# Performance work log

Hardware: AMD Instinct MI355X
Metric: run time of the kernel (lower is better)

## Reference

```python
import jax, jax.numpy as jnp
import numpy as np

N_NODES = 50000
IN_CH = 128
HID_CH = 256
N_EDGES = 800000

def setup_inputs() -> dict:
    key = jax.random.key(0)
    k1, k2, k3, k4, k5 = jax.random.split(key, 5)
    x = jax.random.normal(k1, (N_NODES, IN_CH), dtype=jnp.float32)
    edge_index = jax.random.randint(k2, (2, N_EDGES), 0, N_NODES, dtype=jnp.int64)
    # SAGEConv params: lin_l (applied to aggregated neighbors, has bias), lin_r (applied to root, no bias)
    s = 1.0 / np.sqrt(IN_CH)
    W_l = jax.random.uniform(k3, (IN_CH, HID_CH), dtype=jnp.float32, minval=-s, maxval=s)
    b_l = jnp.zeros((HID_CH,), dtype=jnp.float32)
    W_r = jax.random.uniform(k4, (IN_CH, HID_CH), dtype=jnp.float32, minval=-s, maxval=s)
    return {"x": x, "edge_index": edge_index, "W_l": W_l, "b_l": b_l, "W_r": W_r}

def reference(x, edge_index, W_l, b_l, W_r):
    src, dst = edge_index[0], edge_index[1]
    # gather source features along edges, scatter-mean into destination nodes
    msgs = x[src]  # [E, in]
    agg_sum = jax.ops.segment_sum(msgs, dst, num_segments=N_NODES)  # [N, in]
    deg = jax.ops.segment_sum(jnp.ones((N_EDGES,), x.dtype), dst, num_segments=N_NODES)
    agg = agg_sum / jnp.maximum(deg, 1.0)[:, None]
    # SAGEConv: lin_l(aggregated) + lin_r(root), then ReLU
    out = agg @ W_l + b_l + x @ W_r
    return jax.nn.relu(out)
```

## Files before the change

kernel.cpp:

```cpp
#include <hip/hip_runtime.h>
#include <hip/hip_bf16.h>

#define IN_CH   128
#define HID_CH  256
#define KTOT    256

#define BUCK_NODES 128
#define NBUCK      391
#define BUCK_CAP   2432
#define SCHUNK     4096

typedef __attribute__((ext_vector_type(8))) short bf16x8;
typedef __attribute__((ext_vector_type(4))) float f32x4;
typedef __attribute__((ext_vector_type(2))) float f32x2;

static __device__ __forceinline__ unsigned short f2bf(float f) {
    unsigned int u = __float_as_uint(f);
    unsigned int r = (u + 0x7FFFu + ((u >> 16) & 1u)) >> 16;
    return (unsigned short)r;
}
static __device__ __forceinline__ float bf2f(unsigned int ubits16) {
    return __uint_as_float(ubits16 << 16);
}

static __device__ __forceinline__ void gload_lds16(const void* g, void* l) {
    __builtin_amdgcn_global_load_lds(
        (const __attribute__((address_space(1))) void*)g,
        (__attribute__((address_space(3))) void*)l, 16, 0, 0);
}

static __device__ __forceinline__ unsigned enc_e4m3(float f) {
    unsigned u = __float_as_uint(f);
    unsigned s = (u >> 24) & 0x80u;
    float af = fabsf(f);
    if (af >= 448.f) return s | 0x7Eu;
    if (af < 0.0009765625f) return s;
    if (af < 0.015625f) {
        int m = (int)(af * 512.0f + 0.5f);
        if (m > 7) return s | 0x08u;
        return s | (unsigned)m;
    }
    unsigned au = u & 0x7fffffffu;
    unsigned r = au + 0x0007FFFFu + ((au >> 20) & 1u);
    unsigned e8 = r >> 23;
    unsigned m = (r >> 20) & 7u;
    int e4 = (int)e8 - 120;
    if (e4 >= 16) return s | 0x7Eu;
    return s | ((unsigned)e4 << 3) | m;
}

static __device__ __forceinline__ void dec4_e4m3(unsigned v, float& c0, float& c1,
                                                 float& c2, float& c3) {
#if __has_builtin(__builtin_amdgcn_cvt_pk_f32_fp8)
    f32x2 dlo = __builtin_amdgcn_cvt_pk_f32_fp8(v, false);
    f32x2 dhi = __builtin_amdgcn_cvt_pk_f32_fp8(v, true);
    c0 = dlo.x; c1 = dlo.y; c2 = dhi.x; c3 = dhi.y;
#else
    unsigned b[4] = {v & 0xFFu, (v >> 8) & 0xFFu, (v >> 16) & 0xFFu, v >> 24};
    float o[4];
    #pragma unroll
    for (int i = 0; i < 4; ++i) {
        unsigned e = (b[i] >> 3) & 15u, m = b[i] & 7u;
        unsigned nz = (e != 0u) ? 1u : 0u;
        float val = (float)(m + (nz << 3)) * __uint_as_float((e + 117u + (1u - nz)) << 23);
        o[i] = (b[i] & 0x80u) ? -val : val;
    }
    c0 = o[0]; c1 = o[1]; c2 = o[2]; c3 = o[3];
#endif
}

__global__ __launch_bounds__(1024) void front_kernel(
    const float* __restrict__ x, const int* __restrict__ ei,
    const float* __restrict__ Wl, const float* __restrict__ Wr,
    unsigned short* __restrict__ featb, unsigned char* __restrict__ fx8,
    unsigned short* __restrict__ WT, int* __restrict__ histg,
    int N, int Npad, int E, int nchunk, int nxb)
{
    __shared__ int h[NBUCK];
    const int b = blockIdx.x, tid = threadIdx.x;

    if (b < 64) {
        int t = b * 1024 + tid;
        int n = t >> 8, k = t & 255;
        float v = (k < IN_CH) ? Wl[(size_t)k * HID_CH + n]
                              : Wr[(size_t)(k - IN_CH) * HID_CH + n];
        WT[(size_t)n * KTOT + k] = f2bf(v);
        return;
    }
    if (b < 64 + nxb) {
        int t = (b - 64) * 1024 + tid;
        if (t >= Npad * 16) return;
        int n = t >> 4, c8 = (t & 15) * 8;
        if (n >= N) {
            uint4 z = {0u, 0u, 0u, 0u};
            *reinterpret_cast<uint4*>(featb + (size_t)n * KTOT + c8) = z;
            *reinterpret_cast<uint4*>(featb + (size_t)n * KTOT + IN_CH + c8) = z;
            uint2 z2 = {0u, 0u};
            *reinterpret_cast<uint2*>(fx8 + (size_t)n * IN_CH + c8) = z2;
            return;
        }
        const float* src = x + (size_t)n * IN_CH + c8;
        float4 v0 = *reinterpret_cast<const float4*>(src);
        float4 v1 = *reinterpret_cast<const float4*>(src + 4);
        uint4 o;
        o.x = (unsigned)f2bf(v0.x) | ((unsigned)f2bf(v0.y) << 16);
        o.y = (unsigned)f2bf(v0.z) | ((unsigned)f2bf(v0.w) << 16);
        o.z = (unsigned)f2bf(v1.x) | ((unsigned)f2bf(v1.y) << 16);
        o.w = (unsigned)f2bf(v1.z) | ((unsigned)f2bf(v1.w) << 16);
        *reinterpret_cast<uint4*>(featb + (size_t)n * KTOT + IN_CH + c8) = o;
        uint2 p;
        p.x = enc_e4m3(v0.x) | (enc_e4m3(v0.y) << 8) |
              (enc_e4m3(v0.z) << 16) | (enc_e4m3(v0.w) << 24);
        p.y = enc_e4m3(v1.x) | (enc_e4m3(v1.y) << 8) |
              (enc_e4m3(v1.z) << 16) | (enc_e4m3(v1.w) << 24);
        *reinterpret_cast<uint2*>(fx8 + (size_t)n * IN_CH + c8) = p;
        return;
    }
    int c = b - 64 - nxb;
    if (tid < NBUCK) h[tid] = 0;
    __syncthreads();
    #pragma unroll
    for (int r = 0; r < SCHUNK / 1024; ++r) {
        int i = c * SCHUNK + r * 1024 + tid;
        if (i < E) atomicAdd(&h[((unsigned)ei[E + i]) >> 7], 1);
    }
    __syncthreads();
    if (tid < NBUCK) histg[(size_t)tid * nchunk + c] = h[tid];
}

__global__ __launch_bounds__(1024) void rowscan_kernel(
    int* __restrict__ histg, int* __restrict__ btot, int nchunk)
{
    __shared__ int s[1024];
    const int b = blockIdx.x, t = threadIdx.x;
    int v = (t < nchunk) ? histg[(size_t)b * nchunk + t] : 0;
    s[t] = v;
    __syncthreads();
    #pragma unroll
    for (int off = 1; off < 1024; off <<= 1) {
        int add = (t >= off) ? s[t - off] : 0;
        __syncthreads();
        s[t] += add;
        __syncthreads();
    }
    if (t < nchunk) histg[(size_t)b * nchunk + t] = s[t] - v;
    if (t == 1023) btot[b] = s[1023];
}

__global__ __launch_bounds__(1024) void scatter_part_kernel(
    const int* __restrict__ ei, const int* __restrict__ histg,
    const int* __restrict__ btot, unsigned* __restrict__ barr,
    int E, int nchunk)
{
    __shared__ unsigned stagr[SCHUNK];
    __shared__ unsigned stag[SCHUNK];
    __shared__ unsigned short bidr[SCHUNK];
    __shared__ unsigned short bid[SCHUNK];
    __shared__ int lh[NBUCK];
    __shared__ int lstart[NBUCK];
    __shared__ int lc[NBUCK];
    __shared__ int ls[512];
    __shared__ int sb[512];

    const int c = blockIdx.x, tid = threadIdx.x;
    const int e0 = c * SCHUNK;
    const int nval = min(SCHUNK, E - e0);

    if (tid < NBUCK) lh[tid] = 0;
    if (tid < 512) sb[tid] = (tid < NBUCK) ? btot[tid] : 0;
    __syncthreads();

    #pragma unroll
    for (int r = 0; r < SCHUNK / 1024; ++r) {
        int li = r * 1024 + tid;
        if (li < nval) {
            int i = e0 + li;
            unsigned src = (unsigned)ei[i];
            unsigned dst = (unsigned)ei[E + i];
            unsigned bkt = dst >> 7;
            stagr[li] = src | ((dst & 127u) << 16);
            bidr[li] = (unsigned short)bkt;
            atomicAdd(&lh[bkt], 1);
        }
    }
    __syncthreads();
    #pragma unroll
    for (int off = 1; off < 512; off <<= 1) {
        int add = (tid < 512 && tid >= off) ? sb[tid - off] : 0;
        __syncthreads();
        if (tid < 512) sb[tid] += add;
        __syncthreads();
    }
    if (tid < 512) ls[tid] = (tid < NBUCK) ? lh[tid] : 0;
    __syncthreads();
    #pragma unroll
    for (int off = 1; off < 512; off <<= 1) {
        int add = (tid < 512 && tid >= off) ? ls[tid - off] : 0;
        __syncthreads();
        if (tid < 512) ls[tid] += add;
        __syncthreads();
    }
    if (tid < NBUCK) {
        int st = ls[tid] - lh[tid];
        lstart[tid] = st;
        lc[tid] = 0;
    }
    __syncthreads();

    #pragma unroll
    for (int r = 0; r < SCHUNK / 1024; ++r) {
        int li = r * 1024 + tid;
        if (li < nval) {
            unsigned bkt = bidr[li];
            int pos = lstart[bkt] + atomicAdd(&lc[bkt], 1);
            stag[pos] = stagr[li];
            bid[pos] = (unsigned short)bkt;
        }
    }
    __syncthreads();

    #pragma unroll
    for (int r = 0; r < SCHUNK / 1024; ++r) {
        int li = r * 1024 + tid;
        if (li < nval) {
            unsigned bkt = bid[li];
            int gbase = histg[(size_t)bkt * nchunk + c] +
                        ((bkt == 0) ? 0 : sb[bkt - 1]);
            barr[(size_t)gbase + (li - lstart[bkt])] = stag[li];
        }
    }
}

__global__ __launch_bounds__(1024) void fused_gather_kernel(
    const unsigned* __restrict__ barr, const int* __restrict__ btot,
    const unsigned char* __restrict__ fx8, unsigned short* __restrict__ featb,
    int N)
{
    __shared__ unsigned s_edge[BUCK_CAP];
    __shared__ unsigned short s_col[BUCK_CAP];
    __shared__ int s_cnt[BUCK_NODES];
    __shared__ int s_start[BUCK_NODES];
    __shared__ int s_cur[BUCK_NODES];
    __shared__ int s_scan[BUCK_NODES];
    __shared__ int sb[512];

    const int b = blockIdx.x;
    const int tid = threadIdx.x;
    const int node0 = b * BUCK_NODES;
    const int nnodes = min(BUCK_NODES, N - node0);

    if (tid < 512) sb[tid] = (tid < NBUCK) ? btot[tid] : 0;
    if (tid < BUCK_NODES) s_cnt[tid] = 0;
    __syncthreads();
    #pragma unroll
    for (int off = 1; off < 512; off <<= 1) {
        int add = (tid < 512 && tid >= off) ? sb[tid - off] : 0;
        __syncthreads();
        if (tid < 512) sb[tid] += add;
        __syncthreads();
    }
    const int base = (b == 0) ? 0 : sb[b - 1];
    int nb = btot[b];
    nb = (nb < BUCK_CAP) ? nb : BUCK_CAP;

    for (int i = tid; i < nb; i += 1024) {
        unsigned p = barr[(size_t)base + i];
        s_edge[i] = p;
        atomicAdd(&s_cnt[p >> 16], 1);
    }
    __syncthreads();

    if (tid < BUCK_NODES) s_scan[tid] = s_cnt[tid];
    __syncthreads();
    #pragma unroll
    for (int off = 1; off < BUCK_NODES; off <<= 1) {
        int add = 0;
        if (tid < BUCK_NODES && tid >= off) add = s_scan[tid - off];
        __syncthreads();
        if (tid < BUCK_NODES) s_scan[tid] += add;
        __syncthreads();
    }
    if (tid < BUCK_NODES) {
        int st = s_scan[tid] - s_cnt[tid];
        s_start[tid] = st;
        s_cur[tid] = st;
    }
    __syncthreads();

    for (int i = tid; i < nb; i += 1024) {
        unsigned p = s_edge[i];
        int pos = atomicAdd(&s_cur[p >> 16], 1);
        s_col[pos] = (unsigned short)(p & 0xFFFFu);
    }
    __syncthreads();

    const int wid = tid >> 6, lane = tid & 63;
    const int q4 = lane >> 4, sub = lane & 15;
    for (int pr = wid; pr < BUCK_NODES / 4; pr += 16) {
        int ln = pr * 4 + q4;
        bool live = (ln < nnodes);
        int deg = live ? s_cnt[ln] : 0;
        int beg = live ? s_start[ln] : 0;
        float a0 = 0.f, a1 = 0.f, a2 = 0.f, a3 = 0.f;
        float a4 = 0.f, a5 = 0.f, a6 = 0.f, a7 = 0.f;
        for (int e = 0; e < deg; e += 8) {
            uint2 vv[8];
            #pragma unroll
            for (int q = 0; q < 8; ++q) {
                int ee = e + q;
                ee = (ee < deg) ? ee : (deg - 1);
                int s = s_col[beg + ee];
                vv[q] = *reinterpret_cast<const uint2*>(
                    fx8 + (size_t)s * IN_CH + sub * 8);
            }
            #pragma unroll
            for (int q = 0; q < 8; ++q) {
                float m = (e + q < deg) ? 1.f : 0.f;
                float c0, c1, c2, c3, c4, c5, c6, c7;
                dec4_e4m3(vv[q].x, c0, c1, c2, c3);
                dec4_e4m3(vv[q].y, c4, c5, c6, c7);
                a0 = fmaf(m, c0, a0); a1 = fmaf(m, c1, a1);
                a2 = fmaf(m, c2, a2); a3 = fmaf(m, c3, a3);
                a4 = fmaf(m, c4, a4); a5 = fmaf(m, c5, a5);
                a6 = fmaf(m, c6, a6); a7 = fmaf(m, c7, a7);
            }
        }
        if (live) {
            float inv = 1.0f / fmaxf((float)deg, 1.0f);
            uint4 o;
            o.x = (unsigned)f2bf(a0 * inv) | ((unsigned)f2bf(a1 * inv) << 16);
            o.y = (unsigned)f2bf(a2 * inv) | ((unsigned)f2bf(a3 * inv) << 16);
            o.z = (unsigned)f2bf(a4 * inv) | ((unsigned)f2bf(a5 * inv) << 16);
            o.w = (unsigned)f2bf(a6 * inv) | ((unsigned)f2bf(a7 * inv) << 16);
            *reinterpret_cast<uint4*>(
                featb + (size_t)(node0 + ln) * KTOT + sub * 8) = o;
        }
    }
}

__global__ __launch_bounds__(256, 2) void sage_mfma_kernel(
    const unsigned short* __restrict__ featb,
    const unsigned short* __restrict__ WT,
    const float* __restrict__ bl,
    float* __restrict__ out, int N)
{
    __shared__ unsigned short sA[128][64];
    __shared__ unsigned short sB[256][64];

    const int tid   = threadIdx.x;
    const int nbase = blockIdx.x * 128;
    const int lane  = tid & 63;
    const int w     = tid >> 6;
    const int wr    = (w >> 1) * 64;
    const int wc    = (w & 1) * 128;
    const int lr    = lane & 15;
    const int lk    = (lane >> 4) * 8;
    const int srow  = lane >> 3;
    const int scol  = (lane & 7) * 8;

    f32x4 acc[4][8] = {};

    for (int kb = 0; kb < KTOT; kb += 64) {
        __syncthreads();
        #pragma unroll
        for (int p = 0; p < 4; ++p) {
            int r0 = (w + p * 4) * 8;
            gload_lds16(featb + (size_t)(nbase + r0 + srow) * KTOT + kb + scol,
                        &sA[r0][0]);
        }
        #pragma unroll
        for (int p = 0; p < 8; ++p) {
            int r0 = (w + p * 4) * 8;
            gload_lds16(WT + (size_t)(r0 + srow) * KTOT + kb + scol,
                        &sB[r0][0]);
        }
        __syncthreads();
        #pragma unroll
        for (int ks = 0; ks < 2; ++ks) {
            bf16x8 af[4], bfr[8];
            #pragma unroll
            for (int i = 0; i < 4; ++i)
                af[i] = *reinterpret_cast<const bf16x8*>(&sA[wr + i * 16 + lr][ks * 32 + lk]);
            #pragma unroll
            for (int i = 0; i < 8; ++i)
                bfr[i] = *reinterpret_cast<const bf16x8*>(&sB[wc + i * 16 + lr][ks * 32 + lk]);
            #pragma unroll
            for (int mi = 0; mi < 4; ++mi)
                #pragma unroll
                for (int ni = 0; ni < 8; ++ni)
                    acc[mi][ni] = __builtin_amdgcn_mfma_f32_16x16x32_bf16(
                        af[mi], bfr[ni], acc[mi][ni], 0, 0, 0);
        }
    }

    #pragma unroll
    for (int ni = 0; ni < 8; ++ni) {
        float bias = bl[wc + ni * 16 + lr];
        #pragma unroll
        for (int mi = 0; mi < 4; ++mi) {
            #pragma unroll
            for (int r = 0; r < 4; ++r) {
                int row = nbase + wr + mi * 16 + (lane >> 4) * 4 + r;
                if (row < N) {
                    int colj = wc + ni * 16 + lr;
                    out[(size_t)row * HID_CH + colj] = fmaxf(acc[mi][ni][r] + bias, 0.0f);
                }
            }
        }
    }
}

extern "C" void kernel_launch(void* const* d_in, const int* in_sizes, int n_in,
                              void* d_out, int out_size, void* d_ws, size_t ws_size,
                              hipStream_t stream) {
    const float* x  = (const float*)d_in[0];
    const int*   ei = (const int*)d_in[1];
    const float* Wl = (const float*)d_in[2];
    const float* bl = (const float*)d_in[3];
    const float* Wr = (const float*)d_in[4];
    float* out = (float*)d_out;

    const int N = in_sizes[0] / IN_CH;
    const int E = in_sizes[1] / 2;
    const int Npad   = ((N + 127) / 128) * 128;
    const int nchunk = (E + SCHUNK - 1) / SCHUNK;
    const int nxb    = (Npad * 16 + 1023) / 1024;

    unsigned short* featb = (unsigned short*)d_ws;
    unsigned short* WT    = featb + (size_t)Npad * KTOT;
    unsigned char*  fx8   = (unsigned char*)(WT + KTOT * HID_CH);
    unsigned* barr = (unsigned*)(fx8 + (size_t)Npad * IN_CH);
    int* histg = (int*)(barr + E);
    int* btot  = histg + (size_t)NBUCK * nchunk;

    front_kernel<<<64 + nxb + nchunk, 1024, 0, stream>>>(
        x, ei, Wl, Wr, featb, fx8, WT, histg, N, Npad, E, nchunk, nxb);
    rowscan_kernel<<<NBUCK, 1024, 0, stream>>>(histg, btot, nchunk);
    scatter_part_kernel<<<nchunk, 1024, 0, stream>>>(ei, histg, btot, barr, E, nchunk);
    fused_gather_kernel<<<NBUCK, 1024, 0, stream>>>(barr, btot, fx8, featb, N);
    sage_mfma_kernel<<<Npad / 128, 256, 0, stream>>>(featb, WT, bl, out, N);
}
```

Measured before the change: 79.90 us.

## Replace histogram+rowscan bucket partition with atomic fixed-capacity bucket slots

Removes the per-chunk destination histogram pass and the row-scan kernel, so edges go straight into fixed-capacity per-bucket slots. Each scatter block claims space in a bucket with one global atomicAdd on a per-bucket cursor, which front_kernel zeroes. This cuts one kernel launch, one full read of the destination indices, and the repeated prefix scans over bucket totals. In exchange, edge order within a bucket becomes nondeterministic, and edges beyond BUCK_CAP per bucket are silently dropped, which the code before also truncated.

```diff
diff --git a/kernel.cpp b/kernel.cpp
--- a/kernel.cpp
+++ b/kernel.cpp
@@ -70,16 +70,16 @@
 }
 
 __global__ __launch_bounds__(1024) void front_kernel(
-    const float* __restrict__ x, const int* __restrict__ ei,
+    const float* __restrict__ x,
     const float* __restrict__ Wl, const float* __restrict__ Wr,
     unsigned short* __restrict__ featb, unsigned char* __restrict__ fx8,
-    unsigned short* __restrict__ WT, int* __restrict__ histg,
-    int N, int Npad, int E, int nchunk, int nxb)
+    unsigned short* __restrict__ WT, int* __restrict__ gcur,
+    int N, int Npad)
 {
-    __shared__ int h[NBUCK];
     const int b = blockIdx.x, tid = threadIdx.x;
 
     if (b < 64) {
+        if (b == 0 && tid < NBUCK) gcur[tid] = 0;
         int t = b * 1024 + tid;
         int n = t >> 8, k = t & 255;
         float v = (k < IN_CH) ? Wl[(size_t)k * HID_CH + n]
@@ -87,70 +87,37 @@
         WT[(size_t)n * KTOT + k] = f2bf(v);
         return;
     }
-    if (b < 64 + nxb) {
-        int t = (b - 64) * 1024 + tid;
-        if (t >= Npad * 16) return;
-        int n = t >> 4, c8 = (t & 15) * 8;
-        if (n >= N) {
-            uint4 z = {0u, 0u, 0u, 0u};
-            *reinterpret_cast<uint4*>(featb + (size_t)n * KTOT + c8) = z;
-            *reinterpret_cast<uint4*>(featb + (size_t)n * KTOT + IN_CH + c8) = z;
-            uint2 z2 = {0u, 0u};
-            *reinterpret_cast<uint2*>(fx8 + (size_t)n * IN_CH + c8) = z2;
-            return;
-        }
-        const float* src = x + (size_t)n * IN_CH + c8;
-        float4 v0 = *reinterpret_cast<const float4*>(src);
-        float4 v1 = *reinterpret_cast<const float4*>(src + 4);
-        uint4 o;
-        o.x = (unsigned)f2bf(v0.x) | ((unsigned)f2bf(v0.y) << 16);
-        o.y = (unsigned)f2bf(v0.z) | ((unsigned)f2bf(v0.w) << 16);
-        o.z = (unsigned)f2bf(v1.x) | ((unsigned)f2bf(v1.y) << 16);
-        o.w = (unsigned)f2bf(v1.z) | ((unsigned)f2bf(v1.w) << 16);
-        *reinterpret_cast<uint4*>(featb + (size_t)n * KTOT + IN_CH + c8) = o;
-        uint2 p;
-        p.x = enc_e4m3(v0.x) | (enc_e4m3(v0.y) << 8) |
-              (enc_e4m3(v0.z) << 16) | (enc_e4m3(v0.w) << 24);
-        p.y = enc_e4m3(v1.x) | (enc_e4m3(v1.y) << 8) |
-              (enc_e4m3(v1.z) << 16) | (enc_e4m3(v1.w) << 24);
-        *reinterpret_cast<uint2*>(fx8 + (size_t)n * IN_CH + c8) = p;
+    int t = (b - 64) * 1024 + tid;
+    if (t >= Npad * 16) return;
+    int n = t >> 4, c8 = (t & 15) * 8;
+    if (n >= N) {
+        uint4 z = {0u, 0u, 0u, 0u};
+        *reinterpret_cast<uint4*>(featb + (size_t)n * KTOT + c8) = z;
+        *reinterpret_cast<uint4*>(featb + (size_t)n * KTOT + IN_CH + c8) = z;
+        uint2 z2 = {0u, 0u};
+        *reinterpret_cast<uint2*>(fx8 + (size_t)n * IN_CH + c8) = z2;
         return;
     }
-    int c = b - 64 - nxb;
-    if (tid < NBUCK) h[tid] = 0;
-    __syncthreads();
-    #pragma unroll
-    for (int r = 0; r < SCHUNK / 1024; ++r) {
-        int i = c * SCHUNK + r * 1024 + tid;
-        if (i < E) atomicAdd(&h[((unsigned)ei[E + i]) >> 7], 1);
-    }
-    __syncthreads();
-    if (tid < NBUCK) histg[(size_t)tid * nchunk + c] = h[tid];
-}
-
-__global__ __launch_bounds__(1024) void rowscan_kernel(
-    int* __restrict__ histg, int* __restrict__ btot, int nchunk)
-{
-    __shared__ int s[1024];
-    const int b = blockIdx.x, t = threadIdx.x;
-    int v = (t < nchunk) ? histg[(size_t)b * nchunk + t] : 0;
-    s[t] = v;
-    __syncthreads();
-    #pragma unroll
-    for (int off = 1; off < 1024; off <<= 1) {
-        int add = (t >= off) ? s[t - off] : 0;
-        __syncthreads();
-        s[t] += add;
-        __syncthreads();
-    }
-    if (t < nchunk) histg[(size_t)b * nchunk + t] = s[t] - v;
-    if (t == 1023) btot[b] = s[1023];
+    const float* src = x + (size_t)n * IN_CH + c8;
+    float4 v0 = *reinterpret_cast<const float4*>(src);
+    float4 v1 = *reinterpret_cast<const float4*>(src + 4);
+    uint4 o;
+    o.x = (unsigned)f2bf(v0.x) | ((unsigned)f2bf(v0.y) << 16);
+    o.y = (unsigned)f2bf(v0.z) | ((unsigned)f2bf(v0.w) << 16);
+    o.z = (unsigned)f2bf(v1.x) | ((unsigned)f2bf(v1.y) << 16);
+    o.w = (unsigned)f2bf(v1.z) | ((unsigned)f2bf(v1.w) << 16);
+    *reinterpret_cast<uint4*>(featb + (size_t)n * KTOT + IN_CH + c8) = o;
+    uint2 p;
+    p.x = enc_e4m3(v0.x) | (enc_e4m3(v0.y) << 8) |
+          (enc_e4m3(v0.z) << 16) | (enc_e4m3(v0.w) << 24);
+    p.y = enc_e4m3(v1.x) | (enc_e4m3(v1.y) << 8) |
+          (enc_e4m3(v1.z) << 16) | (enc_e4m3(v1.w) << 24);
+    *reinterpret_cast<uint2*>(fx8 + (size_t)n * IN_CH + c8) = p;
 }
 
 __global__ __launch_bounds__(1024) void scatter_part_kernel(
-    const int* __restrict__ ei, const int* __restrict__ histg,
-    const int* __restrict__ btot, unsigned* __restrict__ barr,
-    int E, int nchunk)
+    const int* __restrict__ ei, int* __restrict__ gcur,
+    unsigned* __restrict__ barr, int E)
 {
     __shared__ unsigned stagr[SCHUNK];
     __shared__ unsigned stag[SCHUNK];
@@ -158,16 +125,15 @@
     __shared__ unsigned short bid[SCHUNK];
     __shared__ int lh[NBUCK];
     __shared__ int lstart[NBUCK];
+    __shared__ int lbase[NBUCK];
     __shared__ int lc[NBUCK];
     __shared__ int ls[512];
-    __shared__ int sb[512];
 
     const int c = blockIdx.x, tid = threadIdx.x;
     const int e0 = c * SCHUNK;
     const int nval = min(SCHUNK, E - e0);
 
     if (tid < NBUCK) lh[tid] = 0;
-    if (tid < 512) sb[tid] = (tid < NBUCK) ? btot[tid] : 0;
     __syncthreads();
 
     #pragma unroll
@@ -184,13 +150,6 @@
         }
     }
     __syncthreads();
-    #pragma unroll
-    for (int off = 1; off < 512; off <<= 1) {
-        int add = (tid < 512 && tid >= off) ? sb[tid - off] : 0;
-        __syncthreads();
-        if (tid < 512) sb[tid] += add;
-        __syncthreads();
-    }
     if (tid < 512) ls[tid] = (tid < NBUCK) ? lh[tid] : 0;
     __syncthreads();
     #pragma unroll
@@ -201,9 +160,10 @@
         __syncthreads();
     }
     if (tid < NBUCK) {
-        int st = ls[tid] - lh[tid];
-        lstart[tid] = st;
+        int cnt = lh[tid];
+        lstart[tid] = ls[tid] - cnt;
         lc[tid] = 0;
+        lbase[tid] = (cnt > 0) ? atomicAdd(&gcur[tid], cnt) : 0;
     }
     __syncthreads();
 
@@ -224,15 +184,15 @@
         int li = r * 1024 + tid;
         if (li < nval) {
             unsigned bkt = bid[li];
-            int gbase = histg[(size_t)bkt * nchunk + c] +
-                        ((bkt == 0) ? 0 : sb[bkt - 1]);
-            barr[(size_t)gbase + (li - lstart[bkt])] = stag[li];
+            int off = lbase[bkt] + (li - lstart[bkt]);
+            if (off < BUCK_CAP)
+                barr[(size_t)bkt * BUCK_CAP + off] = stag[li];
         }
     }
 }
 
 __global__ __launch_bounds__(1024) void fused_gather_kernel(
-    const unsigned* __restrict__ barr, const int* __restrict__ btot,
+    const unsigned* __restrict__ barr, const int* __restrict__ gcur,
     const unsigned char* __restrict__ fx8, unsigned short* __restrict__ featb,
     int N)
 {
@@ -242,29 +202,20 @@
     __shared__ int s_start[BUCK_NODES];
     __shared__ int s_cur[BUCK_NODES];
     __shared__ int s_scan[BUCK_NODES];
-    __shared__ int sb[512];
 
     const int b = blockIdx.x;
     const int tid = threadIdx.x;
     const int node0 = b * BUCK_NODES;
     const int nnodes = min(BUCK_NODES, N - node0);
-
-    if (tid < 512) sb[tid] = (tid < NBUCK) ? btot[tid] : 0;
+    const size_t base = (size_t)b * BUCK_CAP;
+    int nb = gcur[b];
+    nb = (nb < BUCK_CAP) ? nb : BUCK_CAP;
+
     if (tid < BUCK_NODES) s_cnt[tid] = 0;
     __syncthreads();
-    #pragma unroll
-    for (int off = 1; off < 512; off <<= 1) {
-        int add = (tid < 512 && tid >= off) ? sb[tid - off] : 0;
-        __syncthreads();
-        if (tid < 512) sb[tid] += add;
-        __syncthreads();
-    }
-    const int base = (b == 0) ? 0 : sb[b - 1];
-    int nb = btot[b];
-    nb = (nb < BUCK_CAP) ? nb : BUCK_CAP;
 
     for (int i = tid; i < nb; i += 1024) {
-        unsigned p = barr[(size_t)base + i];
+        unsigned p = barr[base + i];
         s_edge[i] = p;
         atomicAdd(&s_cnt[p >> 16], 1);
     }
@@ -430,13 +381,11 @@
     unsigned short* WT    = featb + (size_t)Npad * KTOT;
     unsigned char*  fx8   = (unsigned char*)(WT + KTOT * HID_CH);
     unsigned* barr = (unsigned*)(fx8 + (size_t)Npad * IN_CH);
-    int* histg = (int*)(barr + E);
-    int* btot  = histg + (size_t)NBUCK * nchunk;
-
-    front_kernel<<<64 + nxb + nchunk, 1024, 0, stream>>>(
-        x, ei, Wl, Wr, featb, fx8, WT, histg, N, Npad, E, nchunk, nxb);
-    rowscan_kernel<<<NBUCK, 1024, 0, stream>>>(histg, btot, nchunk);
-    scatter_part_kernel<<<nchunk, 1024, 0, stream>>>(ei, histg, btot, barr, E, nchunk);
-    fused_gather_kernel<<<NBUCK, 1024, 0, stream>>>(barr, btot, fx8, featb, N);
+    int* gcur = (int*)(barr + (size_t)NBUCK * BUCK_CAP);
+
+    front_kernel<<<64 + nxb, 1024, 0, stream>>>(
+        x, Wl, Wr, featb, fx8, WT, gcur, N, Npad);
+    scatter_part_kernel<<<nchunk, 1024, 0, stream>>>(ei, gcur, barr, E);
+    fused_gather_kernel<<<NBUCK, 1024, 0, stream>>>(barr, gcur, fx8, featb, N);
     sage_mfma_kernel<<<Npad / 128, 256, 0, stream>>>(featb, WT, bl, out, N);
 }
```

New measurement: 74.87 us. 6.3% less time.
